# Performance work log

Hardware: AMD Instinct MI355X
Metric: run time of the kernel (lower is better)

The kernel has to match this reference:

```python
import jax, jax.numpy as jnp
import numpy as np

SIZE = 32
NUM_CLASSES = 10
B = 16384
RTOL = 0.01
ATOL = 0.01
MAX_STEPS = 96
H0 = 0.05


def setup_inputs() -> dict:
    key = jax.random.key(0)
    ks = jax.random.split(key, 9)
    p = lambda k, s: 0.1 * jax.random.normal(k, s, dtype=jnp.float32)
    z = lambda n: jnp.zeros((n,), dtype=jnp.float32)
    x = jax.random.normal(ks[0], (B, 2), dtype=jnp.float32)
    # per-sample ODE end times T_i in (0, 3]
    samples = 3.0 * jax.random.uniform(ks[1], (B, 1), dtype=jnp.float32) + 1e-3
    return dict(
        x=x, samples=samples,
        node_w1=p(ks[2], (3, SIZE)), node_b1=z(SIZE),
        node_w2=p(ks[3], (SIZE, SIZE)), node_b2=z(SIZE),
        node_w3=p(ks[4], (SIZE, 2)), node_b3=z(2),
        fc_w=p(ks[5], (2, NUM_CLASSES)), fc_b=z(NUM_CLASSES),
        enc_w1=p(ks[6], (2, SIZE)), enc_b1=z(SIZE),
        enc_w2=p(ks[7], (SIZE, SIZE)), enc_b2=z(SIZE),
        enc_w3=p(ks[8], (SIZE, 2)), enc_b3=z(2),
    )


def _net_forward(x, samples, node_w1, node_b1, node_w2, node_b2, node_w3, node_b3,
                 fc_w, fc_b, enc_w1, enc_b1, enc_w2, enc_b2, enc_w3, enc_b3):
    # Encoder -> (alpha, beta) feed only the external prob_model (no effect on act_vec)
    h = jax.nn.relu(x @ enc_w1 + enc_b1)
    h = jax.nn.relu(h @ enc_w2 + enc_b2)
    ab = h @ enc_w3 + enc_b3
    alpha, beta = jnp.exp(ab[:, 0]), jnp.exp(ab[:, 1])  # unused downstream (side effects only)

    # samples[samples >= 50] = 50
    T = jnp.minimum(samples[:, 0], 50.0)  # [B] per-sample end times

    def f(t, y):  # NODE dynamics; t: [B], y: [B,2]
        zin = jnp.concatenate([t[:, None], y], axis=1)  # [B,3]
        h1 = jax.nn.relu(zin @ node_w1 + node_b1)
        h2 = jax.nn.relu(h1 @ node_w2 + node_b2)
        return h2 @ node_w3 + node_b3  # [B,2]

    def step(carry, _):
        t, y, hstep = carry
        rem = T - t
        active = rem > 1e-8
        hs = jnp.where(active, jnp.minimum(hstep, rem), 0.0)  # never overshoot T
        hb = hs[:, None]
        # Dopri5 (RK45) stages
        k1 = f(t, y)
        k2 = f(t + hs * 0.2, y + hb * (0.2 * k1))
        k3 = f(t + hs * 0.3, y + hb * (3.0 / 40.0 * k1 + 9.0 / 40.0 * k2))
        k4 = f(t + hs * 0.8, y + hb * (44.0 / 45.0 * k1 - 56.0 / 15.0 * k2 + 32.0 / 9.0 * k3))
        k5 = f(t + hs * (8.0 / 9.0), y + hb * (19372.0 / 6561.0 * k1 - 25360.0 / 2187.0 * k2 + 64448.0 / 6561.0 * k3 - 212.0 / 729.0 * k4))
        k6 = f(t + hs, y + hb * (9017.0 / 3168.0 * k1 - 355.0 / 33.0 * k2 + 46732.0 / 5247.0 * k3 + 49.0 / 176.0 * k4 - 5103.0 / 18656.0 * k5))
        y5 = y + hb * (35.0 / 384.0 * k1 + 500.0 / 1113.0 * k3 + 125.0 / 192.0 * k4 - 2187.0 / 6784.0 * k5 + 11.0 / 84.0 * k6)
        k7 = f(t + hs, y5)
        err = hb * (71.0 / 57600.0 * k1 - 71.0 / 16695.0 * k3 + 71.0 / 1920.0 * k4 - 17253.0 / 339200.0 * k5 + 22.0 / 525.0 * k6 - 1.0 / 40.0 * k7)
        scale = ATOL + RTOL * jnp.maximum(jnp.abs(y), jnp.abs(y5))
        en = jnp.sqrt(jnp.mean((err / scale) ** 2, axis=1))  # [B]
        accept = active & (en <= 1.0)
        fac = jnp.clip(0.9 * jnp.maximum(en, 1e-10) ** (-0.2), 0.2, 10.0)
        t_n = jnp.where(accept, t + hs, t)
        y_n = jnp.where(accept[:, None], y5, y)
        h_n = jnp.where(active, hs * fac, hstep)
        return (t_n, y_n, h_n), None

    t0 = jnp.zeros((x.shape[0],), dtype=x.dtype)
    h0 = jnp.full((x.shape[0],), H0, dtype=x.dtype)
    (tF, yF, hF), _ = jax.lax.scan(step, (t0, x, h0), None, length=MAX_STEPS)

    # temp[idx] = flow of x[idx] from t=0 to its own T[idx] (sort/scatter in the
    # original only routes each sample's own interpolated state back to its row)
    act = yF @ fc_w + fc_b  # [B, num_classes]
    return act[None, :, :]  # act_vec: [1, B, num_classes]


def reference(x, samples, node_w1, node_b1, node_w2, node_b2, node_w3, node_b3,
              fc_w, fc_b, enc_w1, enc_b1, enc_w2, enc_b2, enc_w3, enc_b3):
    return _net_forward(x, samples, node_w1, node_b1, node_w2, node_b2, node_w3, node_b3,
                        fc_w, fc_b, enc_w1, enc_b1, enc_w2, enc_b2, enc_w3, enc_b3)
```

## Files before the change

kernel.cpp:

```cpp
#include <hip/hip_runtime.h>
#include <math.h>


#define MAXS 96

typedef float v2f __attribute__((ext_vector_type(2)));

static __device__ __forceinline__ v2f splat(float s) { v2f v; v.x = s; v.y = s; return v; }
static __device__ __forceinline__ v2f vfma(v2f a, v2f b, v2f c) { return __builtin_elementwise_fma(a, b, c); }
static __device__ __forceinline__ v2f vrelu(v2f a) { return __builtin_elementwise_max(a, splat(0.0f)); }

template<int PAT>
static __device__ __forceinline__ float swzf(float x) {
    return __int_as_float(__builtin_amdgcn_ds_swizzle(__float_as_int(x), PAT));
}

#define GPAIR(j) g[2*(j)]   = swzf<(((j) << 5) | 0x10)>(hx); \
                 g[2*(j)+1] = swzf<(((j) << 5) | 0x10)>(hy)

template<int X>
static __device__ __forceinline__ v2f redstage(v2f p) {
    v2f q; q.x = swzf<((X << 10) | 0x1f)>(p.x); q.y = swzf<((X << 10) | 0x1f)>(p.y);
    return p + q;
}

__global__ __launch_bounds__(256, 3) void node_kernel(
    const float* __restrict__ x, const float* __restrict__ samples,
    const float* __restrict__ w1, const float* __restrict__ b1,
    const float* __restrict__ w2, const float* __restrict__ b2,
    const float* __restrict__ w3, const float* __restrict__ b3,
    const float* __restrict__ fcw, const float* __restrict__ fcb,
    float* __restrict__ out, int n)
{
    const int tid  = blockIdx.x * blockDim.x + threadIdx.x;
    const int elem = tid >> 4;
    const int m    = tid & 15;
    if (elem >= n) return;

    const v2f* w1v = (const v2f*)w1;
    const v2f* b1v = (const v2f*)b1;
    const v2f* w2v = (const v2f*)w2;
    const v2f* b2v = (const v2f*)b2;
    const v2f* w3v = (const v2f*)w3;

    v2f w1r0 = w1v[0 * 16 + m];
    v2f w1r1 = w1v[1 * 16 + m];
    v2f w1r2 = w1v[2 * 16 + m];
    v2f b1c  = b1v[m];
    v2f b2c  = b2v[m];
    v2f w3r0 = w3v[2 * m + 0];
    v2f w3r1 = w3v[2 * m + 1];
    v2f b3c  = { b3[0], b3[1] };

    v2f w2c[32];
#pragma unroll
    for (int i = 0; i < 32; ++i) w2c[i] = w2v[i * 16 + m];

#pragma unroll
    for (int i = 0; i < 32; ++i) { asm volatile("" : "+v"(w2c[i])); }
    asm volatile("" : "+v"(w1r0), "+v"(w1r1), "+v"(w1r2), "+v"(b1c), "+v"(b2c));
    asm volatile("" : "+v"(w3r0), "+v"(w3r1));

    v2f y = ((const v2f*)x)[elem];
    float T = fminf(samples[elem], 50.0f);
    float t = 0.0f;
    float h = 0.05f;

    auto f_eval = [&](float tt, v2f z) -> v2f {
        v2f hv = vfma(splat(tt), w1r0, vfma(splat(z.x), w1r1,
                 vfma(splat(z.y), w1r2, b1c)));
        hv = vrelu(hv);
        float hx = hv.x, hy = hv.y;

        float g[32];
        v2f a0 = b2c, a1 = splat(0.0f), a2 = splat(0.0f), a3 = splat(0.0f);

        GPAIR(0);  GPAIR(1);  GPAIR(2);  GPAIR(3);
#pragma unroll
        for (int i = 0; i < 8; ++i)  a0 = vfma(splat(g[i]), w2c[i], a0);
        GPAIR(4);  GPAIR(5);  GPAIR(6);  GPAIR(7);
#pragma unroll
        for (int i = 8; i < 16; ++i) a1 = vfma(splat(g[i]), w2c[i], a1);
        GPAIR(8);  GPAIR(9);  GPAIR(10); GPAIR(11);
#pragma unroll
        for (int i = 16; i < 24; ++i) a2 = vfma(splat(g[i]), w2c[i], a2);
        GPAIR(12); GPAIR(13); GPAIR(14); GPAIR(15);
#pragma unroll
        for (int i = 24; i < 32; ++i) a3 = vfma(splat(g[i]), w2c[i], a3);

        v2f acc = vrelu((a0 + a1) + (a2 + a3));

        v2f p = vfma(splat(acc.x), w3r0, splat(acc.y) * w3r1);
        p = redstage<1>(p);
        p = redstage<2>(p);
        p = redstage<4>(p);
        p = redstage<8>(p);
        return p + b3c;
    };

    v2f k1 = f_eval(0.0f, y);

    for (int s = 0; s < MAXS; ++s) {
        float rem = T - t;
        if (!(rem > 1e-8f)) break;
        float hs = fminf(h, rem);
        v2f hb = splat(hs);

        v2f k2 = f_eval(t + hs * 0.2f, vfma(hb, splat(0.2f) * k1, y));
        v2f k3 = f_eval(t + hs * 0.3f,
                 vfma(hb, vfma(splat((float)(3.0/40.0)), k1, splat((float)(9.0/40.0)) * k2), y));
        v2f k4 = f_eval(t + hs * 0.8f,
                 vfma(hb, vfma(splat((float)(44.0/45.0)), k1,
                          vfma(splat((float)(-56.0/15.0)), k2, splat((float)(32.0/9.0)) * k3)), y));
        v2f k5 = f_eval(t + hs * (float)(8.0/9.0),
                 vfma(hb, vfma(splat((float)(19372.0/6561.0)), k1,
                          vfma(splat((float)(-25360.0/2187.0)), k2,
                          vfma(splat((float)(64448.0/6561.0)), k3,
                               splat((float)(-212.0/729.0)) * k4))), y));
        v2f k6 = f_eval(t + hs,
                 vfma(hb, vfma(splat((float)(9017.0/3168.0)), k1,
                          vfma(splat((float)(-355.0/33.0)), k2,
                          vfma(splat((float)(46732.0/5247.0)), k3,
                          vfma(splat((float)(49.0/176.0)), k4,
                               splat((float)(-5103.0/18656.0)) * k5)))), y));
        v2f y5 = vfma(hb, vfma(splat((float)(35.0/384.0)), k1,
                          vfma(splat((float)(500.0/1113.0)), k3,
                          vfma(splat((float)(125.0/192.0)), k4,
                          vfma(splat((float)(-2187.0/6784.0)), k5,
                               splat((float)(11.0/84.0)) * k6)))), y);
        v2f k7 = f_eval(t + hs, y5);

        v2f err = hb * vfma(splat((float)(71.0/57600.0)), k1,
                       vfma(splat((float)(-71.0/16695.0)), k3,
                       vfma(splat((float)(71.0/1920.0)), k4,
                       vfma(splat((float)(-17253.0/339200.0)), k5,
                       vfma(splat((float)(22.0/525.0)), k6,
                            splat((float)(-1.0/40.0)) * k7)))));

        v2f ay  = __builtin_elementwise_abs(y);
        v2f ay5 = __builtin_elementwise_abs(y5);
        v2f sc  = vfma(splat(0.01f), __builtin_elementwise_max(ay, ay5), splat(0.01f));
        v2f r   = err / sc;
        float en = sqrtf(0.5f * (r.x * r.x + r.y * r.y));

        float fac = 0.9f * powf(fmaxf(en, 1e-10f), -0.2f);
        fac = fminf(fmaxf(fac, 0.2f), 10.0f);

        bool accept = (en <= 1.0f);
        if (accept) { t += hs; y = y5; }
        k1 = accept ? k7 : k1;
        h = hs * fac;
    }

    if (m < 10) {
        out[10 * elem + m] = fmaf(y.x, fcw[m], fmaf(y.y, fcw[10 + m], fcb[m]));
    }
}

extern "C" void kernel_launch(void* const* d_in, const int* in_sizes, int n_in,
                              void* d_out, int out_size, void* d_ws, size_t ws_size,
                              hipStream_t stream) {
    const float* x   = (const float*)d_in[0];
    const float* sm  = (const float*)d_in[1];
    const float* w1  = (const float*)d_in[2];
    const float* b1  = (const float*)d_in[3];
    const float* w2  = (const float*)d_in[4];
    const float* b2  = (const float*)d_in[5];
    const float* w3  = (const float*)d_in[6];
    const float* b3  = (const float*)d_in[7];
    const float* fcw = (const float*)d_in[8];
    const float* fcb = (const float*)d_in[9];
    float* out = (float*)d_out;

    int n = in_sizes[1];
    const int block = 256;
    long long threads = (long long)n * 16;
    int grid = (int)((threads + block - 1) / block);
    node_kernel<<<grid, block, 0, stream>>>(x, sm, w1, b1, w2, b2, w3, b3,
                                            fcw, fcb, out, n);
}
```

Baseline: 110.2 us.

## Broadcast hidden layer via LDS vector reads and reduce with DPP

After: 105.6 us. 1.04x faster.

```diff
diff --git a/kernel.cpp b/kernel.cpp
--- a/kernel.cpp
+++ b/kernel.cpp
@@ -10,18 +10,18 @@
 static __device__ __forceinline__ v2f vfma(v2f a, v2f b, v2f c) { return __builtin_elementwise_fma(a, b, c); }
 static __device__ __forceinline__ v2f vrelu(v2f a) { return __builtin_elementwise_max(a, splat(0.0f)); }
 
-template<int PAT>
-static __device__ __forceinline__ float swzf(float x) {
-    return __int_as_float(__builtin_amdgcn_ds_swizzle(__float_as_int(x), PAT));
+template<int CTRL>
+static __device__ __forceinline__ float dppf(float x) {
+    return __int_as_float(__builtin_amdgcn_update_dpp(
+        0, __float_as_int(x), CTRL, 0xF, 0xF, false));
 }
 
-#define GPAIR(j) g[2*(j)]   = swzf<(((j) << 5) | 0x10)>(hx); \
-                 g[2*(j)+1] = swzf<(((j) << 5) | 0x10)>(hy)
-
-template<int X>
-static __device__ __forceinline__ v2f redstage(v2f p) {
-    v2f q; q.x = swzf<((X << 10) | 0x1f)>(p.x); q.y = swzf<((X << 10) | 0x1f)>(p.y);
-    return p + q;
+static __device__ __forceinline__ v2f dpp_allreduce16(v2f p) {
+    p.x += dppf<0xB1>(p.x);  p.y += dppf<0xB1>(p.y);
+    p.x += dppf<0x4E>(p.x);  p.y += dppf<0x4E>(p.y);
+    p.x += dppf<0x141>(p.x); p.y += dppf<0x141>(p.y);
+    p.x += dppf<0x140>(p.x); p.y += dppf<0x140>(p.y);
+    return p;
 }
 
 __global__ __launch_bounds__(256, 3) void node_kernel(
@@ -36,6 +36,9 @@
     const int elem = tid >> 4;
     const int m    = tid & 15;
     if (elem >= n) return;
+
+    __shared__ float lds[16 * 36];
+    float* slot = &lds[(threadIdx.x >> 4) * 36];
 
     const v2f* w1v = (const v2f*)w1;
     const v2f* b1v = (const v2f*)b1;
@@ -70,31 +73,35 @@
         v2f hv = vfma(splat(tt), w1r0, vfma(splat(z.x), w1r1,
                  vfma(splat(z.y), w1r2, b1c)));
         hv = vrelu(hv);
-        float hx = hv.x, hy = hv.y;
 
-        float g[32];
+        ((v2f*)slot)[m] = hv;
+
+        const float4* gp = (const float4*)slot;
+        float4 r0 = gp[0], r1 = gp[1], r2 = gp[2], r3 = gp[3];
+        float4 r4 = gp[4], r5 = gp[5], r6 = gp[6], r7 = gp[7];
+
         v2f a0 = b2c, a1 = splat(0.0f), a2 = splat(0.0f), a3 = splat(0.0f);
-
-        GPAIR(0);  GPAIR(1);  GPAIR(2);  GPAIR(3);
-#pragma unroll
-        for (int i = 0; i < 8; ++i)  a0 = vfma(splat(g[i]), w2c[i], a0);
-        GPAIR(4);  GPAIR(5);  GPAIR(6);  GPAIR(7);
-#pragma unroll
-        for (int i = 8; i < 16; ++i) a1 = vfma(splat(g[i]), w2c[i], a1);
-        GPAIR(8);  GPAIR(9);  GPAIR(10); GPAIR(11);
-#pragma unroll
-        for (int i = 16; i < 24; ++i) a2 = vfma(splat(g[i]), w2c[i], a2);
-        GPAIR(12); GPAIR(13); GPAIR(14); GPAIR(15);
-#pragma unroll
-        for (int i = 24; i < 32; ++i) a3 = vfma(splat(g[i]), w2c[i], a3);
+        a0 = vfma(splat(r0.x), w2c[ 0], a0); a1 = vfma(splat(r0.y), w2c[ 1], a1);
+        a2 = vfma(splat(r0.z), w2c[ 2], a2); a3 = vfma(splat(r0.w), w2c[ 3], a3);
+        a0 = vfma(splat(r1.x), w2c[ 4], a0); a1 = vfma(splat(r1.y), w2c[ 5], a1);
+        a2 = vfma(splat(r1.z), w2c[ 6], a2); a3 = vfma(splat(r1.w), w2c[ 7], a3);
+        a0 = vfma(splat(r2.x), w2c[ 8], a0); a1 = vfma(splat(r2.y), w2c[ 9], a1);
+        a2 = vfma(splat(r2.z), w2c[10], a2); a3 = vfma(splat(r2.w), w2c[11], a3);
+        a0 = vfma(splat(r3.x), w2c[12], a0); a1 = vfma(splat(r3.y), w2c[13], a1);
+        a2 = vfma(splat(r3.z), w2c[14], a2); a3 = vfma(splat(r3.w), w2c[15], a3);
+        a0 = vfma(splat(r4.x), w2c[16], a0); a1 = vfma(splat(r4.y), w2c[17], a1);
+        a2 = vfma(splat(r4.z), w2c[18], a2); a3 = vfma(splat(r4.w), w2c[19], a3);
+        a0 = vfma(splat(r5.x), w2c[20], a0); a1 = vfma(splat(r5.y), w2c[21], a1);
+        a2 = vfma(splat(r5.z), w2c[22], a2); a3 = vfma(splat(r5.w), w2c[23], a3);
+        a0 = vfma(splat(r6.x), w2c[24], a0); a1 = vfma(splat(r6.y), w2c[25], a1);
+        a2 = vfma(splat(r6.z), w2c[26], a2); a3 = vfma(splat(r6.w), w2c[27], a3);
+        a0 = vfma(splat(r7.x), w2c[28], a0); a1 = vfma(splat(r7.y), w2c[29], a1);
+        a2 = vfma(splat(r7.z), w2c[30], a2); a3 = vfma(splat(r7.w), w2c[31], a3);
 
         v2f acc = vrelu((a0 + a1) + (a2 + a3));
 
         v2f p = vfma(splat(acc.x), w3r0, splat(acc.y) * w3r1);
-        p = redstage<1>(p);
-        p = redstage<2>(p);
-        p = redstage<4>(p);
-        p = redstage<8>(p);
+        p = dpp_allreduce16(p);
         return p + b3c;
     };
 
```
